# Optimization experiments

Hardware: AMD Instinct MI355X
Metric: run time of the kernel (lower is better)

The kernel has to match this reference:

```python
import jax, jax.numpy as jnp
import numpy as np

EPS = 1e-5

def layer_norm(x, g, b):
    mu = jnp.mean(x, axis=-1, keepdims=True)
    var = jnp.mean(jnp.square(x - mu), axis=-1, keepdims=True)
    return (x - mu) * jax.lax.rsqrt(var + EPS) * g + b

def setup_inputs() -> dict:
    key = jax.random.key(0)
    ks = jax.random.split(key, 16)
    B, C, H, W = 32, 128, 56, 56
    D = 64
    s = lambda fan: 1.0 / np.sqrt(fan)
    inp = {
        "x": jax.random.normal(ks[0], (B, C, H, W), dtype=jnp.float32),
        "We": jax.random.uniform(ks[1], (C, D), jnp.float32, -s(C), s(C)),
        "be": jax.random.uniform(ks[2], (D,), jnp.float32, -s(C), s(C)),
        "g1": jnp.ones((D,), jnp.float32), "b1": jnp.zeros((D,), jnp.float32),
        "g2": jnp.ones((D,), jnp.float32), "b2": jnp.zeros((D,), jnp.float32),
        "Wqkv": jax.random.uniform(ks[3], (D, 3 * D), jnp.float32, -s(D), s(D)),
        "bqkv": jax.random.uniform(ks[4], (3 * D,), jnp.float32, -s(D), s(D)),
        "Wp": jax.random.uniform(ks[5], (D, D), jnp.float32, -s(D), s(D)),
        "bp": jax.random.uniform(ks[6], (D,), jnp.float32, -s(D), s(D)),
        "gm": jnp.ones((D,), jnp.float32), "bm": jnp.zeros((D,), jnp.float32),
        "W1": jax.random.uniform(ks[7], (D, D), jnp.float32, -s(D), s(D)),
        "bm1": jax.random.uniform(ks[8], (D,), jnp.float32, -s(D), s(D)),
        "W2": jax.random.uniform(ks[9], (D, D), jnp.float32, -s(D), s(D)),
        "bm2": jax.random.uniform(ks[10], (D,), jnp.float32, -s(D), s(D)),
    }
    return inp

def reference(x, We, be, g1, b1, g2, b2, Wqkv, bqkv, Wp, bp, gm, bm, W1, bm1, W2, bm2):
    B, C, H, W = x.shape
    D = We.shape[1]
    # [B, C, H, W] -> [B, N, C], N = H*W tokens
    t = x.reshape(B, C, H * W).transpose(0, 2, 1)
    t = t @ We + be                                  # embed: [B, N, D]
    t = layer_norm(t, g1, b1)
    t = layer_norm(t, g2, b2)                        # dropout is identity at eval
    qkv = t @ Wqkv + bqkv                            # [B, N, 3D]
    q, k, v = jnp.split(qkv, 3, axis=-1)
    attn = jnp.einsum('bnd,bmd->bnm', q, k) * 0.125  # [B, N, N]
    attn = jax.nn.softmax(attn, axis=-1)
    t = jnp.einsum('bnm,bmd->bnd', attn, v)          # [B, N, D]
    t = t @ Wp + bp                                  # proj (dropout identity)
    h = layer_norm(t, gm, bm)
    h = jax.nn.gelu(h @ W1 + bm1, approximate=False)
    h = h @ W2 + bm2                                 # [B, N, D]
    out = h.transpose(0, 2, 1).reshape(B, D, H, W)
    return jnp.mean(out, axis=1, keepdims=True)      # [B, 1, H, W]
```

## Files before the change

### kernel.cpp

```cpp
#include <hip/hip_runtime.h>
#include <math.h>

#define TB 256
#define NB 32
#define NC 128
#define NHW 3136
#define ND 64
#define NT 49
#define KST 72
#define VST 72

typedef _Float16 half8 __attribute__((ext_vector_type(8)));
typedef _Float16 half4 __attribute__((ext_vector_type(4)));
typedef __fp16 fp16x2 __attribute__((ext_vector_type(2)));
typedef float float4v __attribute__((ext_vector_type(4)));

__device__ __forceinline__ void pack4h(_Float16* dst, float v0, float v1, float v2, float v3){
    union { fp16x2 h[2]; uint2 u; } pk;
    pk.h[0] = __builtin_amdgcn_cvt_pkrtz(v0, v1);
    pk.h[1] = __builtin_amdgcn_cvt_pkrtz(v2, v3);
    *(uint2*)dst = pk.u;
}
__device__ __forceinline__ half4 pack4v(float v0, float v1, float v2, float v3){
    union { fp16x2 h[2]; half4 v; } pk;
    pk.h[0] = __builtin_amdgcn_cvt_pkrtz(v0, v1);
    pk.h[1] = __builtin_amdgcn_cvt_pkrtz(v2, v3);
    return pk.v;
}

__global__ __launch_bounds__(TB) void k_prep(
    const float* __restrict__ We, const float* __restrict__ Wqkv,
    const float* __restrict__ Wp, const float* __restrict__ W1,
    const float* __restrict__ W2, const float* __restrict__ bm2,
    _Float16* __restrict__ WeT, _Float16* __restrict__ WqkvT,
    _Float16* __restrict__ WpT, _Float16* __restrict__ W1T,
    float* __restrict__ w2bx)
{
    const int t = blockIdx.x * TB + threadIdx.x;
    for (int i = t; i < 8192;  i += 2048) WeT[i]   = (_Float16)We[(i & 127) * 64 + (i >> 7)];
    for (int i = t; i < 12288; i += 2048) WqkvT[i] = (_Float16)Wqkv[(i & 63) * 192 + (i >> 6)];
    for (int i = t; i < 4096;  i += 2048) WpT[i]   = (_Float16)Wp[(i & 63) * 64 + (i >> 6)];
    for (int i = t; i < 4096;  i += 2048) W1T[i]   = (_Float16)W1[(i & 63) * 64 + (i >> 6)];
    if (t < 64) {
        float s = 0.f;
        for (int d = 0; d < 64; ++d) s += W2[t * 64 + d];
        w2bx[t] = s * (1.f / 64.f);
    }
    if (t == 64) {
        float s = 0.f;
        for (int d = 0; d < 64; ++d) s += bm2[d];
        w2bx[64] = s * (1.f / 64.f);
    }
}

__global__ __launch_bounds__(TB) void k_embed_qkv(
    const float* __restrict__ x,
    const float* __restrict__ be,
    const float* __restrict__ g1, const float* __restrict__ b1,
    const float* __restrict__ g2, const float* __restrict__ b2,
    const float* __restrict__ bqkv,
    const _Float16* __restrict__ WeT,
    const _Float16* __restrict__ WqkvT,
    _Float16* __restrict__ qh, _Float16* __restrict__ khb, _Float16* __restrict__ vtb)
{
    __shared__ float xs[128 * 66];
    __shared__ _Float16 zL[4 * 16 * 72];
    __shared__ _Float16 vt16[64 * 72];

    const int b = blockIdx.y, n0 = blockIdx.x * 64, tid = threadIdx.x;
    const int w = tid >> 6, lane = tid & 63, quad = lane >> 4, cl = lane & 15;

    {
        const int cb = tid >> 4, tok4 = (tid & 15) * 4;
        const float* xb = x + (size_t)b * NC * NHW + n0 + tok4;
        #pragma unroll
        for (int p = 0; p < 8; ++p) {
            const int c = p * 16 + cb;
            float4 v = *(const float4*)(xb + (size_t)c * NHW);
            float* dst = &xs[c * 66 + tok4];
            *(float2*)dst = make_float2(v.x, v.y);
            *(float2*)(dst + 2) = make_float2(v.z, v.w);
        }
    }
    __syncthreads();

    half8 bx[4];
    #pragma unroll
    for (int ck = 0; ck < 4; ++ck) {
        const float* xp = &xs[(ck * 32 + quad * 8) * 66 + w * 16 + cl];
        union { fp16x2 h[4]; half8 v; } u;
        #pragma unroll
        for (int jj = 0; jj < 4; ++jj)
            u.h[jj] = __builtin_amdgcn_cvt_pkrtz(xp[(2 * jj) * 66], xp[(2 * jj + 1) * 66]);
        bx[ck] = u.v;
    }

    float tv[4][4];
    #pragma unroll
    for (int dt = 0; dt < 4; ++dt) {
        float4 bev = *(const float4*)(be + dt * 16 + quad * 4);
        float4v acc = (float4v){bev.x, bev.y, bev.z, bev.w};
        #pragma unroll
        for (int ck = 0; ck < 4; ++ck) {
            half8 af = *(const half8*)(WeT + (dt * 16 + cl) * 128 + ck * 32 + quad * 8);
            acc = __builtin_amdgcn_mfma_f32_16x16x32_f16(af, bx[ck], acc, 0, 0, 0);
        }
        #pragma unroll
        for (int r = 0; r < 4; ++r) tv[dt][r] = acc[r];
    }

    #pragma unroll
    for (int ln = 0; ln < 2; ++ln) {
        float sm = 0.f;
        #pragma unroll
        for (int dt = 0; dt < 4; ++dt)
            #pragma unroll
            for (int r = 0; r < 4; ++r) sm += tv[dt][r];
        sm += __shfl_xor(sm, 16); sm += __shfl_xor(sm, 32);
        const float mu = sm * (1.f / 64.f);
        float vr = 0.f;
        #pragma unroll
        for (int dt = 0; dt < 4; ++dt)
            #pragma unroll
            for (int r = 0; r < 4; ++r) { float d = tv[dt][r] - mu; vr += d * d; }
        vr += __shfl_xor(vr, 16); vr += __shfl_xor(vr, 32);
        const float is = rsqrtf(vr * (1.f / 64.f) + 1e-5f);
        const float* gp = (ln == 0) ? g1 : g2;
        const float* bp_ = (ln == 0) ? b1 : b2;
        #pragma unroll
        for (int dt = 0; dt < 4; ++dt) {
            float4 gq = *(const float4*)(gp + dt * 16 + quad * 4);
            float4 bq = *(const float4*)(bp_ + dt * 16 + quad * 4);
            const float* gqp = (const float*)&gq;
            const float* bqp = (const float*)&bq;
            #pragma unroll
            for (int r = 0; r < 4; ++r)
                tv[dt][r] = (tv[dt][r] - mu) * is * gqp[r] + bqp[r];
        }
    }

    _Float16* zw = zL + w * (16 * 72);
    #pragma unroll
    for (int dt = 0; dt < 4; ++dt)
        *(half4*)&zw[cl * 72 + dt * 16 + quad * 4] = pack4v(tv[dt][0], tv[dt][1], tv[dt][2], tv[dt][3]);
    __asm__ __volatile__("s_waitcnt lgkmcnt(0)" ::: "memory");
    half8 bz[2];
    #pragma unroll
    for (int ck = 0; ck < 2; ++ck)
        bz[ck] = *(const half8*)&zw[cl * 72 + ck * 32 + quad * 8];

    const float QSC = 0.125f * 1.44269504088896f;
    const int tok = w * 16 + cl;
    #pragma unroll
    for (int et = 0; et < 12; ++et) {
        float4 bq = *(const float4*)(bqkv + et * 16 + quad * 4);
        float4v acc = (float4v){bq.x, bq.y, bq.z, bq.w};
        #pragma unroll
        for (int ck = 0; ck < 2; ++ck) {
            half8 af = *(const half8*)(WqkvT + (et * 16 + cl) * 64 + ck * 32 + quad * 8);
            acc = __builtin_amdgcn_mfma_f32_16x16x32_f16(af, bz[ck], acc, 0, 0, 0);
        }
        if (et < 4) {
            pack4h(qh + ((size_t)(b * NHW + n0 + tok)) * ND + et * 16 + quad * 4,
                   acc[0] * QSC, acc[1] * QSC, acc[2] * QSC, acc[3] * QSC);
        } else if (et < 8) {
            pack4h(khb + ((size_t)(b * NHW + n0 + tok)) * ND + (et - 4) * 16 + quad * 4,
                   acc[0], acc[1], acc[2], acc[3]);
        } else {
            #pragma unroll
            for (int r = 0; r < 4; ++r)
                vt16[((et - 8) * 16 + quad * 4 + r) * 72 + tok] = (_Float16)acc[r];
        }
    }
    __syncthreads();
    #pragma unroll
    for (int i = 0; i < 2; ++i) {
        int ch = tid + 256 * i;
        int row = ch >> 3, off = (ch & 7) * 8;
        *(uint4*)(vtb + ((size_t)(b * ND + row)) * NHW + n0 + off) =
            *(const uint4*)&vt16[row * 72 + off];
    }
}

__global__ __launch_bounds__(TB) void k_attn(
    const _Float16* __restrict__ qh, const _Float16* __restrict__ khb,
    const _Float16* __restrict__ vtb, _Float16* __restrict__ ob)
{
    __shared__ _Float16 Kb[2][64 * KST];
    __shared__ _Float16 Vb[2][64 * VST];

    const int b    = blockIdx.y;
    const int n0   = blockIdx.x * 128;
    const int tid  = threadIdx.x;
    const int w    = tid >> 6;
    const int lane = tid & 63;
    const int quad = lane >> 4;
    const int c    = lane & 15;
    const float CEXP = 4.0f * 1.44269504088896f;

    half8 qf[2][2];
    #pragma unroll
    for (int qt = 0; qt < 2; ++qt) {
        int row = n0 + w * 32 + qt * 16 + c;
        row = row < NHW ? row : NHW - 1;
        const _Float16* qp = qh + ((size_t)(b * NHW + row)) * ND + quad * 8;
        qf[qt][0] = *(const half8*)(qp);
        qf[qt][1] = *(const half8*)(qp + 32);
    }

    float4v o[2][4];
    #pragma unroll
    for (int qt = 0; qt < 2; ++qt)
        #pragma unroll
        for (int nt = 0; nt < 4; ++nt) o[qt][nt] = (float4v){0.f, 0.f, 0.f, 0.f};
    float lp[2] = {0.f, 0.f};

    const _Float16* kbase = khb + ((size_t)b * NHW) * ND;
    const _Float16* vbase = vtb + ((size_t)b * ND) * NHW;

    const int row0 = (tid + 0)   >> 3, off0 = ((tid + 0)   & 7) * 8;
    const int row1 = (tid + 256) >> 3, off1 = ((tid + 256) & 7) * 8;

    uint4 pk0, pk1, pv0, pv1;
    pk0 = *(const uint4*)(kbase + (size_t)row0 * ND + off0);
    pk1 = *(const uint4*)(kbase + (size_t)row1 * ND + off1);
    pv0 = *(const uint4*)(vbase + (size_t)row0 * NHW + off0);
    pv1 = *(const uint4*)(vbase + (size_t)row1 * NHW + off1);

    for (int kt = 0; kt < NT; ++kt) {
        const int bsel = kt & 1;
        __syncthreads();
        *(uint4*)&Kb[bsel][row0 * KST + off0] = pk0;
        *(uint4*)&Kb[bsel][row1 * KST + off1] = pk1;
        *(uint4*)&Vb[bsel][row0 * VST + off0] = pv0;
        *(uint4*)&Vb[bsel][row1 * VST + off1] = pv1;
        if (kt + 1 < NT) {
            const _Float16* kp = kbase + (size_t)((kt + 1) * 64) * ND;
            const _Float16* vp = vbase + (kt + 1) * 64;
            pk0 = *(const uint4*)(kp + (size_t)row0 * ND + off0);
            pk1 = *(const uint4*)(kp + (size_t)row1 * ND + off1);
            pv0 = *(const uint4*)(vp + (size_t)row0 * NHW + off0);
            pv1 = *(const uint4*)(vp + (size_t)row1 * NHW + off1);
        }
        __syncthreads();

        half8 ka[4][2];
        #pragma unroll
        for (int mt = 0; mt < 4; ++mt) {
            const _Float16* kp = &Kb[bsel][(mt * 16 + c) * KST + quad * 8];
            ka[mt][0] = *(const half8*)(kp);
            ka[mt][1] = *(const half8*)(kp + 32);
        }

        float4v s[2][4];
        #pragma unroll
        for (int qt = 0; qt < 2; ++qt)
            #pragma unroll
            for (int mt = 0; mt < 4; ++mt) {
                float4v z = (float4v){-CEXP, -CEXP, -CEXP, -CEXP};
                z = __builtin_amdgcn_mfma_f32_16x16x32_f16(ka[mt][0], qf[qt][0], z, 0, 0, 0);
                z = __builtin_amdgcn_mfma_f32_16x16x32_f16(ka[mt][1], qf[qt][1], z, 0, 0, 0);
                s[qt][mt] = z;
            }

        half4 pb[2][4];
        #pragma unroll
        for (int qt = 0; qt < 2; ++qt) {
            float ls = 0.f;
            #pragma unroll
            for (int mt = 0; mt < 4; ++mt) {
                #pragma unroll
                for (int r = 0; r < 4; ++r) {
                    float p = __builtin_amdgcn_exp2f(s[qt][mt][r]);
                    s[qt][mt][r] = p;
                    ls += p;
                }
                pb[qt][mt] = pack4v(s[qt][mt][0], s[qt][mt][1], s[qt][mt][2], s[qt][mt][3]);
            }
            lp[qt] += ls;
        }

        #pragma unroll
        for (int nt = 0; nt < 4; ++nt) {
            #pragma unroll
            for (int mt = 0; mt < 4; ++mt) {
                half4 vv = *(const half4*)&Vb[bsel][(nt * 16 + c) * VST + mt * 16 + quad * 4];
                #pragma unroll
                for (int qt = 0; qt < 2; ++qt)
                    o[qt][nt] = __builtin_amdgcn_mfma_f32_16x16x16f16(vv, pb[qt][mt], o[qt][nt], 0, 0, 0);
            }
        }
    }

    #pragma unroll
    for (int qt = 0; qt < 2; ++qt) {
        float lq = lp[qt];
        lq += __shfl_xor(lq, 16); lq += __shfl_xor(lq, 32);
        float inv = 1.f / lq;
        int row = n0 + w * 32 + qt * 16 + c;
        if (row < NHW) {
            _Float16* op = ob + ((size_t)(b * NHW + row)) * ND + quad * 4;
            #pragma unroll
            for (int nt = 0; nt < 4; ++nt)
                pack4h(op + nt * 16, o[qt][nt][0] * inv, o[qt][nt][1] * inv,
                       o[qt][nt][2] * inv, o[qt][nt][3] * inv);
        }
    }
}

__global__ __launch_bounds__(TB) void k_post(
    const _Float16* __restrict__ aih,
    const float* __restrict__ bp,
    const float* __restrict__ gm, const float* __restrict__ bm,
    const float* __restrict__ bm1,
    const _Float16* __restrict__ WpT, const _Float16* __restrict__ W1T,
    const float* __restrict__ w2bx,
    float* __restrict__ out)
{
    __shared__ _Float16 zL2[4 * 16 * 72];

    const int b = blockIdx.y, n0 = blockIdx.x * 64, tid = threadIdx.x;
    const int w = tid >> 6, lane = tid & 63, quad = lane >> 4, cl = lane & 15;
    const int tok = w * 16 + cl;

    const _Float16* ap = aih + ((size_t)(b * NHW + n0 + tok)) * ND;
    half8 ba[2];
    ba[0] = *(const half8*)(ap + quad * 8);
    ba[1] = *(const half8*)(ap + 32 + quad * 8);

    float uv[4][4];
    #pragma unroll
    for (int et = 0; et < 4; ++et) {
        float4 bq = *(const float4*)(bp + et * 16 + quad * 4);
        float4v acc = (float4v){bq.x, bq.y, bq.z, bq.w};
        #pragma unroll
        for (int ck = 0; ck < 2; ++ck) {
            half8 af = *(const half8*)(WpT + (et * 16 + cl) * 64 + ck * 32 + quad * 8);
            acc = __builtin_amdgcn_mfma_f32_16x16x32_f16(af, ba[ck], acc, 0, 0, 0);
        }
        #pragma unroll
        for (int r = 0; r < 4; ++r) uv[et][r] = acc[r];
    }

    {
        float sm = 0.f;
        #pragma unroll
        for (int et = 0; et < 4; ++et)
            #pragma unroll
            for (int r = 0; r < 4; ++r) sm += uv[et][r];
        sm += __shfl_xor(sm, 16); sm += __shfl_xor(sm, 32);
        const float mu = sm * (1.f / 64.f);
        float vr = 0.f;
        #pragma unroll
        for (int et = 0; et < 4; ++et)
            #pragma unroll
            for (int r = 0; r < 4; ++r) { float d = uv[et][r] - mu; vr += d * d; }
        vr += __shfl_xor(vr, 16); vr += __shfl_xor(vr, 32);
        const float is = rsqrtf(vr * (1.f / 64.f) + 1e-5f);
        #pragma unroll
        for (int et = 0; et < 4; ++et) {
            float4 gq = *(const float4*)(gm + et * 16 + quad * 4);
            float4 bq = *(const float4*)(bm + et * 16 + quad * 4);
            const float* gqp = (const float*)&gq;
            const float* bqp = (const float*)&bq;
            #pragma unroll
            for (int r = 0; r < 4; ++r)
                uv[et][r] = (uv[et][r] - mu) * is * gqp[r] + bqp[r];
        }
    }

    _Float16* zw = zL2 + w * (16 * 72);
    #pragma unroll
    for (int et = 0; et < 4; ++et)
        *(half4*)&zw[cl * 72 + et * 16 + quad * 4] = pack4v(uv[et][0], uv[et][1], uv[et][2], uv[et][3]);
    __asm__ __volatile__("s_waitcnt lgkmcnt(0)" ::: "memory");
    half8 bz[2];
    #pragma unroll
    for (int ck = 0; ck < 2; ++ck)
        bz[ck] = *(const half8*)&zw[cl * 72 + ck * 32 + quad * 8];

    float part = 0.f;
    #pragma unroll
    for (int et = 0; et < 4; ++et) {
        float4 b1q = *(const float4*)(bm1 + et * 16 + quad * 4);
        float4v acc = (float4v){b1q.x, b1q.y, b1q.z, b1q.w};
        #pragma unroll
        for (int ck = 0; ck < 2; ++ck) {
            half8 af = *(const half8*)(W1T + (et * 16 + cl) * 64 + ck * 32 + quad * 8);
            acc = __builtin_amdgcn_mfma_f32_16x16x32_f16(af, bz[ck], acc, 0, 0, 0);
        }
        float4 wq = *(const float4*)(w2bx + et * 16 + quad * 4);
        const float* wqp = (const float*)&wq;
        #pragma unroll
        for (int r = 0; r < 4; ++r) {
            float h = acc[r];
            float g = 0.5f * h * (1.f + erff(h * 0.70710678118654752f));
            part = fmaf(g, wqp[r], part);
        }
    }
    part += __shfl_xor(part, 16); part += __shfl_xor(part, 32);
    if (lane < 16)
        out[(size_t)b * NHW + n0 + tok] = part + w2bx[64];
}

extern "C" void kernel_launch(void* const* d_in, const int* in_sizes, int n_in,
                              void* d_out, int out_size, void* d_ws, size_t ws_size,
                              hipStream_t stream) {
    (void)in_sizes; (void)n_in; (void)out_size; (void)ws_size;
    const float* x    = (const float*)d_in[0];
    const float* We   = (const float*)d_in[1];
    const float* be   = (const float*)d_in[2];
    const float* g1   = (const float*)d_in[3];
    const float* b1   = (const float*)d_in[4];
    const float* g2   = (const float*)d_in[5];
    const float* b2   = (const float*)d_in[6];
    const float* Wqkv = (const float*)d_in[7];
    const float* bqkv = (const float*)d_in[8];
    const float* Wp   = (const float*)d_in[9];
    const float* bp   = (const float*)d_in[10];
    const float* gm   = (const float*)d_in[11];
    const float* bm   = (const float*)d_in[12];
    const float* W1   = (const float*)d_in[13];
    const float* bm1  = (const float*)d_in[14];
    const float* W2   = (const float*)d_in[15];
    const float* bm2  = (const float*)d_in[16];
    float* out = (float*)d_out;

    const size_t NQ = (size_t)NB * NHW * ND;
    _Float16* qh    = (_Float16*)d_ws;
    _Float16* khb   = qh + NQ;
    _Float16* vtb   = khb + NQ;
    _Float16* obf   = vtb + NQ;
    _Float16* WeT   = obf + NQ;
    _Float16* WqkvT = WeT + 64 * 128;
    _Float16* WpT   = WqkvT + 192 * 64;
    _Float16* W1T   = WpT + 64 * 64;
    float*    w2bx  = (float*)(W1T + 64 * 64);

    dim3 blk(TB);
    k_prep<<<dim3(8), blk, 0, stream>>>(We, Wqkv, Wp, W1, W2, bm2, WeT, WqkvT, WpT, W1T, w2bx);
    k_embed_qkv<<<dim3(NT, NB), blk, 0, stream>>>(x, be, g1, b1, g2, b2, bqkv, WeT, WqkvT, qh, khb, vtb);
    k_attn<<<dim3(25, NB), blk, 0, stream>>>(qh, khb, vtb, obf);
    k_post<<<dim3(NT, NB), blk, 0, stream>>>(obf, bp, gm, bm, bm1, WpT, W1T, w2bx, out);
}
```

Measured before the change: 318.6 us.

## Give each attention warp 64 queries with 128-thread blocks; shrink embed LDS

The attention kernel now runs 128-thread blocks of two warps, and each warp handles 64 query rows instead of 32. Every K/V fragment loaded from shared memory then feeds twice as many MFMAs, cutting LDS traffic per unit of work. Each thread now stages four K and four V chunks per tile instead of two. Register pressure rises and there are half as many waves per block (launch bounds set to 2 blocks minimum). Separately, the embed kernel stages x in LDS as fp16 instead of fp32 and reuses that buffer for the V transpose, which shrinks its shared memory footprint and may raise occupancy but adds an extra barrier.

```diff
diff --git a/kernel.cpp b/kernel.cpp
--- a/kernel.cpp
+++ b/kernel.cpp
@@ -2,6 +2,7 @@
 #include <math.h>
 
 #define TB 256
+#define ATB 128
 #define NB 32
 #define NC 128
 #define NHW 3136
@@ -63,9 +64,8 @@
     const _Float16* __restrict__ WqkvT,
     _Float16* __restrict__ qh, _Float16* __restrict__ khb, _Float16* __restrict__ vtb)
 {
-    __shared__ float xs[128 * 66];
+    __shared__ __align__(16) _Float16 xsm[128 * 68];
     __shared__ _Float16 zL[4 * 16 * 72];
-    __shared__ _Float16 vt16[64 * 72];
 
     const int b = blockIdx.y, n0 = blockIdx.x * 64, tid = threadIdx.x;
     const int w = tid >> 6, lane = tid & 63, quad = lane >> 4, cl = lane & 15;
@@ -77,9 +77,7 @@
         for (int p = 0; p < 8; ++p) {
             const int c = p * 16 + cb;
             float4 v = *(const float4*)(xb + (size_t)c * NHW);
-            float* dst = &xs[c * 66 + tok4];
-            *(float2*)dst = make_float2(v.x, v.y);
-            *(float2*)(dst + 2) = make_float2(v.z, v.w);
+            pack4h(&xsm[c * 68 + tok4], v.x, v.y, v.z, v.w);
         }
     }
     __syncthreads();
@@ -87,13 +85,13 @@
     half8 bx[4];
     #pragma unroll
     for (int ck = 0; ck < 4; ++ck) {
-        const float* xp = &xs[(ck * 32 + quad * 8) * 66 + w * 16 + cl];
-        union { fp16x2 h[4]; half8 v; } u;
-        #pragma unroll
-        for (int jj = 0; jj < 4; ++jj)
-            u.h[jj] = __builtin_amdgcn_cvt_pkrtz(xp[(2 * jj) * 66], xp[(2 * jj + 1) * 66]);
+        const _Float16* xp = &xsm[(ck * 32 + quad * 8) * 68 + w * 16 + cl];
+        union { _Float16 h[8]; half8 v; } u;
+        #pragma unroll
+        for (int jj = 0; jj < 8; ++jj) u.h[jj] = xp[jj * 68];
         bx[ck] = u.v;
     }
+    __syncthreads();
 
     float tv[4][4];
     #pragma unroll
@@ -149,6 +147,7 @@
     for (int ck = 0; ck < 2; ++ck)
         bz[ck] = *(const half8*)&zw[cl * 72 + ck * 32 + quad * 8];
 
+    _Float16* vt16 = xsm;
     const float QSC = 0.125f * 1.44269504088896f;
     const int tok = w * 16 + cl;
     #pragma unroll
@@ -182,7 +181,7 @@
     }
 }
 
-__global__ __launch_bounds__(TB) void k_attn(
+__global__ __launch_bounds__(ATB, 2) void k_attn(
     const _Float16* __restrict__ qh, const _Float16* __restrict__ khb,
     const _Float16* __restrict__ vtb, _Float16* __restrict__ ob)
 {
@@ -198,49 +197,52 @@
     const int c    = lane & 15;
     const float CEXP = 4.0f * 1.44269504088896f;
 
-    half8 qf[2][2];
-    #pragma unroll
-    for (int qt = 0; qt < 2; ++qt) {
-        int row = n0 + w * 32 + qt * 16 + c;
+    half8 qf[4][2];
+    #pragma unroll
+    for (int qt = 0; qt < 4; ++qt) {
+        int row = n0 + w * 64 + qt * 16 + c;
         row = row < NHW ? row : NHW - 1;
         const _Float16* qp = qh + ((size_t)(b * NHW + row)) * ND + quad * 8;
         qf[qt][0] = *(const half8*)(qp);
         qf[qt][1] = *(const half8*)(qp + 32);
     }
 
-    float4v o[2][4];
-    #pragma unroll
-    for (int qt = 0; qt < 2; ++qt)
+    float4v o[4][4];
+    #pragma unroll
+    for (int qt = 0; qt < 4; ++qt)
         #pragma unroll
         for (int nt = 0; nt < 4; ++nt) o[qt][nt] = (float4v){0.f, 0.f, 0.f, 0.f};
-    float lp[2] = {0.f, 0.f};
+    float lp[4] = {0.f, 0.f, 0.f, 0.f};
 
     const _Float16* kbase = khb + ((size_t)b * NHW) * ND;
     const _Float16* vbase = vtb + ((size_t)b * ND) * NHW;
 
-    const int row0 = (tid + 0)   >> 3, off0 = ((tid + 0)   & 7) * 8;
-    const int row1 = (tid + 256) >> 3, off1 = ((tid + 256) & 7) * 8;
-
-    uint4 pk0, pk1, pv0, pv1;
-    pk0 = *(const uint4*)(kbase + (size_t)row0 * ND + off0);
-    pk1 = *(const uint4*)(kbase + (size_t)row1 * ND + off1);
-    pv0 = *(const uint4*)(vbase + (size_t)row0 * NHW + off0);
-    pv1 = *(const uint4*)(vbase + (size_t)row1 * NHW + off1);
+    const int rowA = tid >> 3;
+    const int offA = (tid & 7) * 8;
+
+    uint4 pk[4], pv[4];
+    #pragma unroll
+    for (int i = 0; i < 4; ++i) {
+        pk[i] = *(const uint4*)(kbase + (size_t)(rowA + 16 * i) * ND + offA);
+        pv[i] = *(const uint4*)(vbase + (size_t)(rowA + 16 * i) * NHW + offA);
+    }
 
     for (int kt = 0; kt < NT; ++kt) {
         const int bsel = kt & 1;
         __syncthreads();
-        *(uint4*)&Kb[bsel][row0 * KST + off0] = pk0;
-        *(uint4*)&Kb[bsel][row1 * KST + off1] = pk1;
-        *(uint4*)&Vb[bsel][row0 * VST + off0] = pv0;
-        *(uint4*)&Vb[bsel][row1 * VST + off1] = pv1;
+        #pragma unroll
+        for (int i = 0; i < 4; ++i) {
+            *(uint4*)&Kb[bsel][(rowA + 16 * i) * KST + offA] = pk[i];
+            *(uint4*)&Vb[bsel][(rowA + 16 * i) * VST + offA] = pv[i];
+        }
         if (kt + 1 < NT) {
             const _Float16* kp = kbase + (size_t)((kt + 1) * 64) * ND;
             const _Float16* vp = vbase + (kt + 1) * 64;
-            pk0 = *(const uint4*)(kp + (size_t)row0 * ND + off0);
-            pk1 = *(const uint4*)(kp + (size_t)row1 * ND + off1);
-            pv0 = *(const uint4*)(vp + (size_t)row0 * NHW + off0);
-            pv1 = *(const uint4*)(vp + (size_t)row1 * NHW + off1);
+            #pragma unroll
+            for (int i = 0; i < 4; ++i) {
+                pk[i] = *(const uint4*)(kp + (size_t)(rowA + 16 * i) * ND + offA);
+                pv[i] = *(const uint4*)(vp + (size_t)(rowA + 16 * i) * NHW + offA);
+            }
         }
         __syncthreads();
 
@@ -252,32 +254,28 @@
             ka[mt][1] = *(const half8*)(kp + 32);
         }
 
-        float4v s[2][4];
-        #pragma unroll
-        for (int qt = 0; qt < 2; ++qt)
+        half4 pb[4][4];
+        #pragma unroll
+        for (int qt = 0; qt < 4; ++qt) {
+            float4v s[4];
             #pragma unroll
             for (int mt = 0; mt < 4; ++mt) {
                 float4v z = (float4v){-CEXP, -CEXP, -CEXP, -CEXP};
                 z = __builtin_amdgcn_mfma_f32_16x16x32_f16(ka[mt][0], qf[qt][0], z, 0, 0, 0);
                 z = __builtin_amdgcn_mfma_f32_16x16x32_f16(ka[mt][1], qf[qt][1], z, 0, 0, 0);
-                s[qt][mt] = z;
+                s[mt] = z;
             }
-
-        half4 pb[2][4];
-        #pragma unroll
-        for (int qt = 0; qt < 2; ++qt) {
-            float ls = 0.f;
+            float pm[4];
             #pragma unroll
             for (int mt = 0; mt < 4; ++mt) {
-                #pragma unroll
-                for (int r = 0; r < 4; ++r) {
-                    float p = __builtin_amdgcn_exp2f(s[qt][mt][r]);
-                    s[qt][mt][r] = p;
-                    ls += p;
-                }
-                pb[qt][mt] = pack4v(s[qt][mt][0], s[qt][mt][1], s[qt][mt][2], s[qt][mt][3]);
+                float p0 = __builtin_amdgcn_exp2f(s[mt][0]);
+                float p1 = __builtin_amdgcn_exp2f(s[mt][1]);
+                float p2 = __builtin_amdgcn_exp2f(s[mt][2]);
+                float p3 = __builtin_amdgcn_exp2f(s[mt][3]);
+                pb[qt][mt] = pack4v(p0, p1, p2, p3);
+                pm[mt] = (p0 + p1) + (p2 + p3);
             }
-            lp[qt] += ls;
+            lp[qt] += (pm[0] + pm[1]) + (pm[2] + pm[3]);
         }
 
         #pragma unroll
@@ -286,18 +284,18 @@
             for (int mt = 0; mt < 4; ++mt) {
                 half4 vv = *(const half4*)&Vb[bsel][(nt * 16 + c) * VST + mt * 16 + quad * 4];
                 #pragma unroll
-                for (int qt = 0; qt < 2; ++qt)
+                for (int qt = 0; qt < 4; ++qt)
                     o[qt][nt] = __builtin_amdgcn_mfma_f32_16x16x16f16(vv, pb[qt][mt], o[qt][nt], 0, 0, 0);
             }
         }
     }
 
     #pragma unroll
-    for (int qt = 0; qt < 2; ++qt) {
+    for (int qt = 0; qt < 4; ++qt) {
         float lq = lp[qt];
         lq += __shfl_xor(lq, 16); lq += __shfl_xor(lq, 32);
         float inv = 1.f / lq;
-        int row = n0 + w * 32 + qt * 16 + c;
+        int row = n0 + w * 64 + qt * 16 + c;
         if (row < NHW) {
             _Float16* op = ob + ((size_t)(b * NHW + row)) * ND + quad * 4;
             #pragma unroll
@@ -440,6 +438,6 @@
     dim3 blk(TB);
     k_prep<<<dim3(8), blk, 0, stream>>>(We, Wqkv, Wp, W1, W2, bm2, WeT, WqkvT, WpT, W1T, w2bx);
     k_embed_qkv<<<dim3(NT, NB), blk, 0, stream>>>(x, be, g1, b1, g2, b2, bqkv, WeT, WqkvT, qh, khb, vtb);
-    k_attn<<<dim3(25, NB), blk, 0, stream>>>(qh, khb, vtb, obf);
+    k_attn<<<dim3(25, NB), dim3(ATB), 0, stream>>>(qh, khb, vtb, obf);
     k_post<<<dim3(NT, NB), blk, 0, stream>>>(obf, bp, gm, bm, bm1, WpT, W1T, w2bx, out);
 }
```

Measured after the change: 424.2 us. +33.2%, slower.
